# Optimization experiments

Measured on AMD Instinct MI355X. Metric: run time of the kernel, lower is better.

The kernel has to match this reference:

```python
import jax, jax.numpy as jnp
import numpy as np

EPS = 1e-3  # Keras BatchNormalization default epsilon
B = 4096
TX = 32
SUB = 13


def setup_inputs() -> dict:
    key = jax.random.key(0)
    ks = jax.random.split(key, 24)
    f32 = jnp.float32
    n = lambda k, s: jax.random.normal(k, s, dtype=f32)
    u = lambda k, s: jax.random.uniform(k, s, dtype=f32)
    W_SCALE = jnp.float32(0.05)  # keras truncated_normal default stddev
    inp = {
        'V1': n(ks[0], (B, TX, SUB, 2)),
        'V2': n(ks[1], (B, TX, SUB, 2)),
        'W1': n(ks[2], (2, 64, 1024)) * W_SCALE,
        'b1': n(ks[3], (2, 1024)) * W_SCALE,
        'g1': u(ks[4], (2, 1024)) + jnp.float32(0.5),
        'be1': n(ks[5], (2, 1024)) * jnp.float32(0.1),
        'm1': n(ks[6], (2, 1024)) * jnp.float32(0.1),
        'v1': u(ks[7], (2, 1024)) + jnp.float32(0.5),
        'W2': n(ks[8], (2, 1024, 512)) * W_SCALE,
        'b2': n(ks[9], (2, 512)) * W_SCALE,
        'g2': u(ks[10], (2, 512)) + jnp.float32(0.5),
        'be2': n(ks[11], (2, 512)) * jnp.float32(0.1),
        'm2': n(ks[12], (2, 512)) * jnp.float32(0.1),
        'v2': u(ks[13], (2, 512)) + jnp.float32(0.5),
        'W3': n(ks[14], (2, 512, 512)) * W_SCALE,
        'b3': n(ks[15], (2, 512)) * W_SCALE,
        'g3': u(ks[16], (2, 512)) + jnp.float32(0.5),
        'be3': n(ks[17], (2, 512)) * jnp.float32(0.1),
        'm3': n(ks[18], (2, 512)) * jnp.float32(0.1),
        'v3': u(ks[19], (2, 512)) + jnp.float32(0.5),
        'W4': n(ks[20], (2, 512, 64)) * W_SCALE,
        'b4': n(ks[21], (2, 64)) * W_SCALE,
    }
    return inp


def _dense_bn_relu(x, W, b, g, be, m, v):
    # Dense(activation='relu') followed by BatchNormalization (inference mode),
    # batched over the tower dim t in {real, imag}.
    h = jax.nn.relu(jnp.einsum('tbi,tio->tbo', x, W) + b[:, None, :])
    return (h - m[:, None, :]) * (g[:, None, :] * jax.lax.rsqrt(v[:, None, :] + EPS)) + be[:, None, :]


def reference(V1, V2, W1, b1, g1, be1, m1, v1, W2, b2, g2, be2, m2, v2,
              W3, b3, g3, be3, m3, v3, W4, b4):
    # Per-UE input normalization over (tx, real/imag) per subband
    def norm_in(V):
        return V / jnp.sqrt(jnp.sum(V * V, axis=(1, 3), keepdims=True))

    inp = jnp.concatenate([norm_in(V1), norm_in(V2)], axis=1)  # (B, 2*TX, SUB, 2)
    b = inp.shape[0]
    # Vectorize the 13-subband python loop: (B, 64, SUB, 2) -> (2 towers, B*SUB, 64)
    x = jnp.transpose(inp, (3, 0, 2, 1)).reshape(2, b * SUB, 2 * TX)

    h = _dense_bn_relu(x, W1, b1, g1, be1, m1, v1)
    h = _dense_bn_relu(h, W2, b2, g2, be2, m2, v2)
    h = _dense_bn_relu(h, W3, b3, g3, be3, m3, v3)
    z = jnp.einsum('tbi,tio->tbo', h, W4) + b4[:, None, :]  # (2, B*SUB, 64)

    V_r = z[0].reshape(b, SUB, TX, 2)                   # linear head (real tower)
    V_i = jax.nn.sigmoid(z[1]).reshape(b, SUB, TX, 2)   # sigmoid head (imag tower)

    # Per-subband, per-UE joint L2 normalization over the 32 tx antennas
    nrm = jnp.sqrt(jnp.sum(V_r * V_r + V_i * V_i, axis=2, keepdims=True))  # (B, SUB, 1, 2)
    V_r = V_r / nrm
    V_i = V_i / nrm

    # C2R + transpose per UE: (B, SUB, TX) complex -> (B, TX, SUB, 2) real
    def per_ue(u):
        return jnp.transpose(jnp.stack([V_r[..., u], V_i[..., u]], axis=-1), (0, 2, 1, 3))

    mix_V = jnp.concatenate([per_ue(0), per_ue(1)], axis=1)  # (B, 2*TX, SUB, 2)
    return mix_V
```

## Files before the change

kernel.cpp:

```cpp
#include <hip/hip_runtime.h>
#include <hip/hip_bf16.h>

typedef __attribute__((ext_vector_type(8))) short bf16x8;
typedef __attribute__((ext_vector_type(4))) float f32x4;

#define GLOAD16(gsrc, ldst)                                                    \
  __builtin_amdgcn_global_load_lds(                                            \
      (const __attribute__((address_space(1))) unsigned int*)(const void*)(gsrc), \
      (__attribute__((address_space(3))) unsigned int*)(void*)(ldst), 16, 0, 0)

static constexpr int    MROWS = 53248;
static constexpr size_t M64   = (size_t)MROWS * 64;

__global__ void transpose_w(const float* __restrict__ W, __hip_bfloat16* __restrict__ Wt,
                            int K, int N) {
  int total = 2 * K * N;
  int idx = blockIdx.x * 256 + threadIdx.x;
  if (idx >= total) return;
  int t   = idx / (K * N);
  int rem = idx - t * K * N;
  int n   = rem / K;
  int k   = rem - n * K;
  Wt[idx] = __float2bfloat16(W[(size_t)t * K * N + (size_t)k * N + n]);
}

__global__ void bn_prep(const float* __restrict__ g, const float* __restrict__ be,
                        const float* __restrict__ m, const float* __restrict__ v,
                        float* __restrict__ s, float* __restrict__ o, int n) {
  int i = blockIdx.x * 256 + threadIdx.x;
  if (i < n) {
    float sc = g[i] * rsqrtf(v[i] + 1e-3f);
    s[i] = sc;
    o[i] = be[i] - m[i] * sc;
  }
}

__global__ __launch_bounds__(256) void input_norm(const float* __restrict__ V1,
                                                  const float* __restrict__ V2,
                                                  __hip_bfloat16* __restrict__ x) {
  __shared__ float lv[1664];
  __shared__ float inv_s[26];
  const int b = blockIdx.x, tid = threadIdx.x;
  for (int idx = tid; idx < 1664; idx += 256)
    lv[idx] = (idx < 832) ? V1[(size_t)b * 832 + idx] : V2[(size_t)b * 832 + idx - 832];
  __syncthreads();
  if (tid < 26) {
    int ue = tid / 13, s = tid - ue * 13;
    const float* base = &lv[ue * 832 + s * 2];
    float sum = 0.f;
#pragma unroll
    for (int tx = 0; tx < 32; ++tx) {
      float a = base[tx * 26], c = base[tx * 26 + 1];
      sum += a * a + c * c;
    }
    inv_s[tid] = rsqrtf(sum);
  }
  __syncthreads();
  for (int idx = tid; idx < 1664; idx += 256) {
    int t = idx / 832, rem = idx - t * 832;
    int s = rem >> 6, c = rem & 63;
    int ue = c >> 5, tx = c & 31;
    float val = lv[ue * 832 + tx * 26 + s * 2 + t] * inv_s[ue * 13 + s];
    x[(size_t)t * M64 + (size_t)(b * 13 + s) * 64 + c] = __float2bfloat16(val);
  }
}

template <int N, int K, int BN, int ACT>
__global__ __launch_bounds__(256) void gemm_db(const __hip_bfloat16* __restrict__ A,
                                               size_t strideA, int aRow0,
                                               const __hip_bfloat16* __restrict__ Wt,
                                               const float* __restrict__ bias,
                                               const float* __restrict__ sc,
                                               const float* __restrict__ ofs,
                                               __hip_bfloat16* __restrict__ Y,
                                               float* __restrict__ Z,
                                               size_t strideO, int nby) {
  constexpr int BM = 128, BK = 64;
  constexpr int GX = N / BN;
  constexpr int MI = 4, NI = BN / 32;
  constexpr int AI = (BM * BK) / (256 * 8);
  constexpr int BI = (BN * BK) / (256 * 8);
  constexpr int NT = K / BK;
  __shared__ __align__(16) __hip_bfloat16 lsA[2][BM * BK];
  __shared__ __align__(16) __hip_bfloat16 lsB[2][BN * BK];

  const int nwg = GX * nby * 2;
  const int L   = blockIdx.x;
  const int q = nwg >> 3, r = nwg & 7;
  const int xcd = L & 7, idx = L >> 3;
  const int wg = (xcd < r ? xcd * (q + 1) : r * (q + 1) + (xcd - r) * q) + idx;
  const int t   = wg / (GX * nby);
  const int rem = wg - t * (GX * nby);
  const int by  = rem / GX;
  const int bx  = rem - by * GX;
  const int m0 = by * BM, n0 = bx * BN;

  const int tid = threadIdx.x;
  const int lane = tid & 63, wave = tid >> 6;
  const int wr = wave >> 1, wc = wave & 1;
  const int l15 = lane & 15, lhi = lane >> 4;

  const __hip_bfloat16* Ab = A + (size_t)t * strideA;
  const __hip_bfloat16* Wb = Wt + (size_t)t * N * K;

  f32x4 acc[MI][NI];
#pragma unroll
  for (int i = 0; i < MI; ++i)
#pragma unroll
    for (int j = 0; j < NI; ++j) acc[i][j] = (f32x4){0.f, 0.f, 0.f, 0.f};

  auto stage = [&](int buf, int k0) {
#pragma unroll
    for (int c = 0; c < AI; ++c) {
      int e = (c * 256 + tid) * 8;
      GLOAD16(&Ab[(size_t)(aRow0 + m0 + (e >> 6)) * K + k0 + (e & 63)],
              &lsA[buf][(c * 256 + wave * 64) * 8]);
    }
#pragma unroll
    for (int c = 0; c < BI; ++c) {
      int e = (c * 256 + tid) * 8;
      GLOAD16(&Wb[(size_t)(n0 + (e >> 6)) * K + k0 + (e & 63)],
              &lsB[buf][(c * 256 + wave * 64) * 8]);
    }
  };

  auto compute = [&](int buf) {
#pragma unroll
    for (int kk = 0; kk < 2; ++kk) {
      bf16x8 af[MI], bfr[NI];
#pragma unroll
      for (int i = 0; i < MI; ++i)
        af[i] = *(const bf16x8*)&lsA[buf][(wr * 64 + i * 16 + l15) * BK + kk * 32 + lhi * 8];
#pragma unroll
      for (int j = 0; j < NI; ++j)
        bfr[j] = *(const bf16x8*)&lsB[buf][(wc * (BN / 2) + j * 16 + l15) * BK + kk * 32 + lhi * 8];
#pragma unroll
      for (int i = 0; i < MI; ++i)
#pragma unroll
        for (int j = 0; j < NI; ++j)
          acc[i][j] = __builtin_amdgcn_mfma_f32_16x16x32_bf16(af[i], bfr[j], acc[i][j], 0, 0, 0);
    }
  };

  stage(0, 0);
  __syncthreads();
  int cur = 0;
  for (int kt = 0; kt < NT - 1; ++kt) {
    stage(cur ^ 1, (kt + 1) * BK);
    compute(cur);
    __syncthreads();
    cur ^= 1;
  }
  compute(cur);

  const int gcb = n0 + wc * (BN / 2) + l15;
  float bi[NI], si[NI], oi[NI];
#pragma unroll
  for (int j = 0; j < NI; ++j) {
    int gc = gcb + j * 16;
    bi[j] = bias[t * N + gc];
    if constexpr (ACT) {
      si[j] = sc[t * N + gc];
      oi[j] = ofs[t * N + gc];
    }
  }
#pragma unroll
  for (int i = 0; i < MI; ++i) {
    int grow = m0 + wr * 64 + i * 16 + lhi * 4;
#pragma unroll
    for (int j = 0; j < NI; ++j) {
      int gc = gcb + j * 16;
#pragma unroll
      for (int rr = 0; rr < 4; ++rr) {
        float val = acc[i][j][rr] + bi[j];
        if constexpr (ACT) {
          val = fmaxf(val, 0.f) * si[j] + oi[j];
          Y[(size_t)t * strideO + (size_t)(grow + rr) * N + gc] = __float2bfloat16(val);
        } else {
          Z[(size_t)t * strideO + (size_t)(grow + rr) * N + gc] = val;
        }
      }
    }
  }
}

__global__ __launch_bounds__(256) void postproc(const float* __restrict__ Z,
                                                size_t zstride, int row0,
                                                float* __restrict__ out) {
  const int zrow = blockIdx.x * 4 + (threadIdx.x >> 6);
  const int o = threadIdx.x & 63;
  float zr = Z[(size_t)zrow * 64 + o];
  float zl = Z[zstride + (size_t)zrow * 64 + o];
  float vi = 1.f / (1.f + expf(-zl));
  float p = zr * zr + vi * vi;
  p += __shfl_xor(p, 2);
  p += __shfl_xor(p, 4);
  p += __shfl_xor(p, 8);
  p += __shfl_xor(p, 16);
  p += __shfl_xor(p, 32);
  float inv = rsqrtf(p);
  int grow = row0 + zrow;
  int bb = grow / 13, s = grow - bb * 13;
  int tx = o >> 1, ue = o & 1;
  size_t base = (((size_t)bb * 64 + ue * 32 + tx) * 13 + s) * 2;
  out[base]     = zr * inv;
  out[base + 1] = vi * inv;
}

extern "C" void kernel_launch(void* const* d_in, const int* in_sizes, int n_in,
                              void* d_out, int out_size, void* d_ws, size_t ws_size,
                              hipStream_t stream) {
  const float* V1 = (const float*)d_in[0];
  const float* V2 = (const float*)d_in[1];
  const float* W1 = (const float*)d_in[2];
  const float* b1 = (const float*)d_in[3];
  const float* g1 = (const float*)d_in[4];
  const float* be1 = (const float*)d_in[5];
  const float* m1 = (const float*)d_in[6];
  const float* v1 = (const float*)d_in[7];
  const float* W2 = (const float*)d_in[8];
  const float* b2 = (const float*)d_in[9];
  const float* g2 = (const float*)d_in[10];
  const float* be2 = (const float*)d_in[11];
  const float* m2 = (const float*)d_in[12];
  const float* v2 = (const float*)d_in[13];
  const float* W3 = (const float*)d_in[14];
  const float* b3 = (const float*)d_in[15];
  const float* g3 = (const float*)d_in[16];
  const float* be3 = (const float*)d_in[17];
  const float* m3 = (const float*)d_in[18];
  const float* v3 = (const float*)d_in[19];
  const float* W4 = (const float*)d_in[20];
  const float* b4 = (const float*)d_in[21];
  float* out = (float*)d_out;

  char* ws = (char*)d_ws;
  constexpr size_t OFF_WT1 = 0;
  constexpr size_t OFF_WT2 = OFF_WT1 + 262144;
  constexpr size_t OFF_WT3 = OFF_WT2 + 2097152;
  constexpr size_t OFF_WT4 = OFF_WT3 + 1048576;
  constexpr size_t OFF_S1  = OFF_WT4 + 131072;
  constexpr size_t OFF_O1  = OFF_S1 + 8192;
  constexpr size_t OFF_S2  = OFF_O1 + 8192;
  constexpr size_t OFF_O2  = OFF_S2 + 4096;
  constexpr size_t OFF_S3  = OFF_O2 + 4096;
  constexpr size_t OFF_O3  = OFF_S3 + 4096;
  constexpr size_t OFF_X   = OFF_O3 + 4096;
  constexpr size_t FIXED_END = OFF_X + 13631488;

  __hip_bfloat16* wt1 = (__hip_bfloat16*)(ws + OFF_WT1);
  __hip_bfloat16* wt2 = (__hip_bfloat16*)(ws + OFF_WT2);
  __hip_bfloat16* wt3 = (__hip_bfloat16*)(ws + OFF_WT3);
  __hip_bfloat16* wt4 = (__hip_bfloat16*)(ws + OFF_WT4);
  float* s1 = (float*)(ws + OFF_S1);
  float* o1 = (float*)(ws + OFF_O1);
  float* s2 = (float*)(ws + OFF_S2);
  float* o2 = (float*)(ws + OFF_O2);
  float* s3 = (float*)(ws + OFF_S3);
  float* o3 = (float*)(ws + OFF_O3);
  __hip_bfloat16* xb = (__hip_bfloat16*)(ws + OFF_X);

  constexpr int TOT_BLOCKS = 416;
  size_t avail = (ws_size > FIXED_END) ? (ws_size - FIXED_END) : 0;
  long sb = (long)(avail / ((size_t)8704 * 128));
  int seg_blocks = (sb < 1) ? 1 : (sb > TOT_BLOCKS ? TOT_BLOCKS : (int)sb);
  const int seg_rows = seg_blocks * 128;
  const size_t H1E = (size_t)seg_rows * 1024;
  const size_t H2E = (size_t)seg_rows * 512;
  const size_t ZE  = (size_t)seg_rows * 64;
  const size_t OFF_H1 = FIXED_END;
  const size_t OFF_H2 = OFF_H1 + 2 * H1E * 2;
  const size_t OFF_H3 = OFF_H2 + 2 * H2E * 2;
  const size_t OFF_Z  = OFF_H3 + 2 * H2E * 2;
  __hip_bfloat16* h1 = (__hip_bfloat16*)(ws + OFF_H1);
  __hip_bfloat16* h2 = (__hip_bfloat16*)(ws + OFF_H2);
  __hip_bfloat16* h3 = (__hip_bfloat16*)(ws + OFF_H3);
  float*          zb = (float*)(ws + OFF_Z);

  transpose_w<<<(2 * 64 * 1024 + 255) / 256, 256, 0, stream>>>(W1, wt1, 64, 1024);
  transpose_w<<<(2 * 1024 * 512 + 255) / 256, 256, 0, stream>>>(W2, wt2, 1024, 512);
  transpose_w<<<(2 * 512 * 512 + 255) / 256, 256, 0, stream>>>(W3, wt3, 512, 512);
  transpose_w<<<(2 * 512 * 64 + 255) / 256, 256, 0, stream>>>(W4, wt4, 512, 64);
  bn_prep<<<8, 256, 0, stream>>>(g1, be1, m1, v1, s1, o1, 2048);
  bn_prep<<<4, 256, 0, stream>>>(g2, be2, m2, v2, s2, o2, 1024);
  bn_prep<<<4, 256, 0, stream>>>(g3, be3, m3, v3, s3, o3, 1024);

  input_norm<<<4096, 256, 0, stream>>>(V1, V2, xb);

  for (int bl0 = 0; bl0 < TOT_BLOCKS; bl0 += seg_blocks) {
    int nb = (TOT_BLOCKS - bl0 < seg_blocks) ? (TOT_BLOCKS - bl0) : seg_blocks;
    int r0 = bl0 * 128;
    gemm_db<1024, 64, 128, 1><<<8 * nb * 2, 256, 0, stream>>>(
        xb, M64, r0, wt1, b1, s1, o1, h1, nullptr, H1E, nb);
    gemm_db<512, 1024, 128, 1><<<4 * nb * 2, 256, 0, stream>>>(
        h1, H1E, 0, wt2, b2, s2, o2, h2, nullptr, H2E, nb);
    gemm_db<512, 512, 128, 1><<<4 * nb * 2, 256, 0, stream>>>(
        h2, H2E, 0, wt3, b3, s3, o3, h3, nullptr, H2E, nb);
    gemm_db<64, 512, 64, 0><<<1 * nb * 2, 256, 0, stream>>>(
        h3, H2E, 0, wt4, b4, nullptr, nullptr, nullptr, zb, ZE, nb);
    postproc<<<nb * 32, 256, 0, stream>>>(zb, ZE, r0, out);
  }

  (void)in_sizes; (void)n_in; (void)out_size;
}
```

Before: 564.8 us.

## Add 256x256 eight-wave GEMM with XOR-swizzled LDS for layers two and three

Adds a new GEMM kernel with 256x256 tiles over 8 waves that interleaves global-to-LDS prefetch of the next K tile with MFMA phases, using barriers and s_setprio to pace them. It is used for the two large hidden layers. LDS tiles in both kernels now use an XOR column swizzle to avoid bank conflicts on the fragment reads. Segment block counts are forced even so the 256-row tiles divide evenly. The larger tiles cut global traffic per FLOP but need 128 KB of LDS and many accumulator registers, which limits occupancy and could spill.

New measurement: 454.5 us. 1.24x faster.

```diff
diff --git a/kernel.cpp b/kernel.cpp
--- a/kernel.cpp
+++ b/kernel.cpp
@@ -63,6 +63,157 @@
     float val = lv[ue * 832 + tx * 26 + s * 2 + t] * inv_s[ue * 13 + s];
     x[(size_t)t * M64 + (size_t)(b * 13 + s) * 64 + c] = __float2bfloat16(val);
   }
+}
+
+__device__ __forceinline__ int xcd_swz(int L, int nwg) {
+  int q = nwg >> 3, r = nwg & 7;
+  int xcd = L & 7, idx = L >> 3;
+  return (xcd < r ? xcd * (q + 1) : r * (q + 1) + (xcd - r) * q) + idx;
+}
+
+template <int N, int K, int ACT>
+__global__ __launch_bounds__(512, 2) void gemm_8p(const __hip_bfloat16* __restrict__ A,
+                                                  size_t strideA, int aRow0,
+                                                  const __hip_bfloat16* __restrict__ Wt,
+                                                  const float* __restrict__ bias,
+                                                  const float* __restrict__ sc,
+                                                  const float* __restrict__ ofs,
+                                                  __hip_bfloat16* __restrict__ Y,
+                                                  float* __restrict__ Z,
+                                                  size_t strideO, int nby) {
+  constexpr int BK = 64;
+  constexpr int GX = N / 256;
+  constexpr int NT = K / BK;
+  __shared__ __align__(16) __hip_bfloat16 lds[2][2][256 * 64];
+
+  const int nwg = GX * nby * 2;
+  const int wg = xcd_swz(blockIdx.x, nwg);
+  const int t   = wg / (GX * nby);
+  const int rem = wg - t * (GX * nby);
+  const int by  = rem / GX;
+  const int bx  = rem - by * GX;
+  const int m0 = by * 256, n0 = bx * 256;
+
+  const int tid = threadIdx.x;
+  const int lane = tid & 63, wave = tid >> 6;
+  const int wr = wave >> 2, wc = wave & 3;
+  const int l15 = lane & 15, lhi = lane >> 4;
+
+  const __hip_bfloat16* Ab = A + (size_t)t * strideA;
+  const __hip_bfloat16* Wb = Wt + (size_t)t * N * K;
+
+  f32x4 acc[8][4];
+#pragma unroll
+  for (int i = 0; i < 8; ++i)
+#pragma unroll
+    for (int j = 0; j < 4; ++j) acc[i][j] = (f32x4){0.f, 0.f, 0.f, 0.f};
+
+  auto stage_half = [&](int buf, int k0, int h) {
+#pragma unroll
+    for (int c = 0; c < 2; ++c) {
+      int e = (c * 512 + tid) * 8;
+      int rl = e >> 6;
+      int col = (e & 63) ^ ((rl & 7) << 3);
+      const __hip_bfloat16* src =
+          (h < 2) ? &Ab[(size_t)(aRow0 + m0 + h * 128 + rl) * K + k0 + col]
+                  : &Wb[(size_t)(n0 + (h - 2) * 128 + rl) * K + k0 + col];
+      GLOAD16(src, &lds[buf][h >> 1][((h & 1) * 128) * 64 + (c * 512 + wave * 64) * 8]);
+    }
+  };
+  auto ldA = [&](int buf, int mi, int kk) {
+    int ra = wr * 128 + mi * 16 + l15;
+    return *(const bf16x8*)&lds[buf][0][ra * 64 + ((kk * 32 + lhi * 8) ^ ((l15 & 7) << 3))];
+  };
+  auto ldB = [&](int buf, int ni, int kk) {
+    int rb = wc * 64 + ni * 16 + l15;
+    return *(const bf16x8*)&lds[buf][1][rb * 64 + ((kk * 32 + lhi * 8) ^ ((l15 & 7) << 3))];
+  };
+
+#pragma unroll
+  for (int h = 0; h < 4; ++h) stage_half(0, 0, h);
+  asm volatile("s_waitcnt vmcnt(0)" ::: "memory");
+  __builtin_amdgcn_s_barrier();
+
+  for (int T = 0; T < NT; ++T) {
+    const int cur = T & 1, nxt = cur ^ 1;
+    const int k1 = (T + 1) * BK;
+    const bool pf = (T + 1 < NT);
+    bf16x8 a0[8], b0, b1;
+
+#pragma unroll
+    for (int mi = 0; mi < 8; ++mi) a0[mi] = ldA(cur, mi, 0);
+    b0 = ldB(cur, 0, 0); b1 = ldB(cur, 1, 0);
+    if (pf) { stage_half(nxt, k1, 0); stage_half(nxt, k1, 1); }
+    __builtin_amdgcn_s_barrier();
+    __builtin_amdgcn_s_setprio(1);
+#pragma unroll
+    for (int mi = 0; mi < 8; ++mi) {
+      acc[mi][0] = __builtin_amdgcn_mfma_f32_16x16x32_bf16(a0[mi], b0, acc[mi][0], 0, 0, 0);
+      acc[mi][1] = __builtin_amdgcn_mfma_f32_16x16x32_bf16(a0[mi], b1, acc[mi][1], 0, 0, 0);
+    }
+    __builtin_amdgcn_s_setprio(0);
+
+    b0 = ldB(cur, 2, 0); b1 = ldB(cur, 3, 0);
+    if (pf) { stage_half(nxt, k1, 2); stage_half(nxt, k1, 3); }
+    __builtin_amdgcn_s_barrier();
+    __builtin_amdgcn_s_setprio(1);
+#pragma unroll
+    for (int mi = 0; mi < 8; ++mi) {
+      acc[mi][2] = __builtin_amdgcn_mfma_f32_16x16x32_bf16(a0[mi], b0, acc[mi][2], 0, 0, 0);
+      acc[mi][3] = __builtin_amdgcn_mfma_f32_16x16x32_bf16(a0[mi], b1, acc[mi][3], 0, 0, 0);
+    }
+    __builtin_amdgcn_s_setprio(0);
+
+#pragma unroll
+    for (int mi = 0; mi < 8; ++mi) a0[mi] = ldA(cur, mi, 1);
+    b0 = ldB(cur, 0, 1); b1 = ldB(cur, 1, 1);
+    __builtin_amdgcn_s_barrier();
+    __builtin_amdgcn_s_setprio(1);
+#pragma unroll
+    for (int mi = 0; mi < 8; ++mi) {
+      acc[mi][0] = __builtin_amdgcn_mfma_f32_16x16x32_bf16(a0[mi], b0, acc[mi][0], 0, 0, 0);
+      acc[mi][1] = __builtin_amdgcn_mfma_f32_16x16x32_bf16(a0[mi], b1, acc[mi][1], 0, 0, 0);
+    }
+    __builtin_amdgcn_s_setprio(0);
+
+    b0 = ldB(cur, 2, 1); b1 = ldB(cur, 3, 1);
+    __builtin_amdgcn_s_barrier();
+    __builtin_amdgcn_s_setprio(1);
+#pragma unroll
+    for (int mi = 0; mi < 8; ++mi) {
+      acc[mi][2] = __builtin_amdgcn_mfma_f32_16x16x32_bf16(a0[mi], b0, acc[mi][2], 0, 0, 0);
+      acc[mi][3] = __builtin_amdgcn_mfma_f32_16x16x32_bf16(a0[mi], b1, acc[mi][3], 0, 0, 0);
+    }
+    __builtin_amdgcn_s_setprio(0);
+
+    asm volatile("s_waitcnt vmcnt(0)" ::: "memory");
+    __builtin_amdgcn_s_barrier();
+  }
+
+  const int gcb = n0 + wc * 64 + l15;
+  float bi[4], si[4], oi[4];
+#pragma unroll
+  for (int j = 0; j < 4; ++j) {
+    int gc = gcb + j * 16;
+    bi[j] = bias[t * N + gc];
+    si[j] = sc[t * N + gc];
+    oi[j] = ofs[t * N + gc];
+  }
+#pragma unroll
+  for (int mi = 0; mi < 8; ++mi) {
+    int grow = m0 + wr * 128 + mi * 16 + lhi * 4;
+#pragma unroll
+    for (int j = 0; j < 4; ++j) {
+      int gc = gcb + j * 16;
+#pragma unroll
+      for (int rr = 0; rr < 4; ++rr) {
+        float val = acc[mi][j][rr] + bi[j];
+        val = fmaxf(val, 0.f) * si[j] + oi[j];
+        Y[(size_t)t * strideO + (size_t)(grow + rr) * N + gc] = __float2bfloat16(val);
+      }
+    }
+  }
+  (void)Z;
 }
 
 template <int N, int K, int BN, int ACT>
@@ -85,10 +236,7 @@
   __shared__ __align__(16) __hip_bfloat16 lsB[2][BN * BK];
 
   const int nwg = GX * nby * 2;
-  const int L   = blockIdx.x;
-  const int q = nwg >> 3, r = nwg & 7;
-  const int xcd = L & 7, idx = L >> 3;
-  const int wg = (xcd < r ? xcd * (q + 1) : r * (q + 1) + (xcd - r) * q) + idx;
+  const int wg = xcd_swz(blockIdx.x, nwg);
   const int t   = wg / (GX * nby);
   const int rem = wg - t * (GX * nby);
   const int by  = rem / GX;
@@ -113,13 +261,15 @@
 #pragma unroll
     for (int c = 0; c < AI; ++c) {
       int e = (c * 256 + tid) * 8;
-      GLOAD16(&Ab[(size_t)(aRow0 + m0 + (e >> 6)) * K + k0 + (e & 63)],
+      int col = (e & 63) ^ (((e >> 6) & 7) << 3);
+      GLOAD16(&Ab[(size_t)(aRow0 + m0 + (e >> 6)) * K + k0 + col],
               &lsA[buf][(c * 256 + wave * 64) * 8]);
     }
 #pragma unroll
     for (int c = 0; c < BI; ++c) {
       int e = (c * 256 + tid) * 8;
-      GLOAD16(&Wb[(size_t)(n0 + (e >> 6)) * K + k0 + (e & 63)],
+      int col = (e & 63) ^ (((e >> 6) & 7) << 3);
+      GLOAD16(&Wb[(size_t)(n0 + (e >> 6)) * K + k0 + col],
               &lsB[buf][(c * 256 + wave * 64) * 8]);
     }
   };
@@ -130,10 +280,12 @@
       bf16x8 af[MI], bfr[NI];
 #pragma unroll
       for (int i = 0; i < MI; ++i)
-        af[i] = *(const bf16x8*)&lsA[buf][(wr * 64 + i * 16 + l15) * BK + kk * 32 + lhi * 8];
+        af[i] = *(const bf16x8*)&lsA[buf][(wr * 64 + i * 16 + l15) * BK +
+                                          ((kk * 32 + lhi * 8) ^ ((l15 & 7) << 3))];
 #pragma unroll
       for (int j = 0; j < NI; ++j)
-        bfr[j] = *(const bf16x8*)&lsB[buf][(wc * (BN / 2) + j * 16 + l15) * BK + kk * 32 + lhi * 8];
+        bfr[j] = *(const bf16x8*)&lsB[buf][(wc * (BN / 2) + j * 16 + l15) * BK +
+                                           ((kk * 32 + lhi * 8) ^ ((l15 & 7) << 3))];
 #pragma unroll
       for (int i = 0; i < MI; ++i)
 #pragma unroll
@@ -263,7 +415,8 @@
   constexpr int TOT_BLOCKS = 416;
   size_t avail = (ws_size > FIXED_END) ? (ws_size - FIXED_END) : 0;
   long sb = (long)(avail / ((size_t)8704 * 128));
-  int seg_blocks = (sb < 1) ? 1 : (sb > TOT_BLOCKS ? TOT_BLOCKS : (int)sb);
+  int seg_blocks = (sb < 2) ? 2 : (sb > TOT_BLOCKS ? TOT_BLOCKS : (int)sb);
+  seg_blocks &= ~1;
   const int seg_rows = seg_blocks * 128;
   const size_t H1E = (size_t)seg_rows * 1024;
   const size_t H2E = (size_t)seg_rows * 512;
@@ -290,12 +443,13 @@
   for (int bl0 = 0; bl0 < TOT_BLOCKS; bl0 += seg_blocks) {
     int nb = (TOT_BLOCKS - bl0 < seg_blocks) ? (TOT_BLOCKS - bl0) : seg_blocks;
     int r0 = bl0 * 128;
+    int nby8 = nb / 2;
     gemm_db<1024, 64, 128, 1><<<8 * nb * 2, 256, 0, stream>>>(
         xb, M64, r0, wt1, b1, s1, o1, h1, nullptr, H1E, nb);
-    gemm_db<512, 1024, 128, 1><<<4 * nb * 2, 256, 0, stream>>>(
-        h1, H1E, 0, wt2, b2, s2, o2, h2, nullptr, H2E, nb);
-    gemm_db<512, 512, 128, 1><<<4 * nb * 2, 256, 0, stream>>>(
-        h2, H2E, 0, wt3, b3, s3, o3, h3, nullptr, H2E, nb);
+    gemm_8p<512, 1024, 1><<<2 * nby8 * 2, 512, 0, stream>>>(
+        h1, H1E, 0, wt2, b2, s2, o2, h2, nullptr, H2E, nby8);
+    gemm_8p<512, 512, 1><<<2 * nby8 * 2, 512, 0, stream>>>(
+        h2, H2E, 0, wt3, b3, s3, o3, h3, nullptr, H2E, nby8);
     gemm_db<64, 512, 64, 0><<<1 * nb * 2, 256, 0, stream>>>(
         h3, H2E, 0, wt4, b4, nullptr, nullptr, nullptr, zb, ZE, nb);
     postproc<<<nb * 32, 256, 0, stream>>>(zb, ZE, r0, out);
```
